# Kernel optimization log

Measured on AMD Instinct MI355X. Metric: run time of the kernel, lower is better.

Reference implementation:

```python
import jax, jax.numpy as jnp
import numpy as np

D_OUT, D_IN, NOBJ, H, A = 12, 2, 8, 256, 100
BN_EPS = 1e-5
N_TOK = 16384  # = 2048 scenes * 8 objects


def _lin(x, W, b=None):
    y = x @ W.T
    return y + b if b is not None else y


def _bn1(x, gamma, beta):
    # BatchNorm1d(num_features=1) in training mode: single channel ->
    # batch statistics are taken over every element of the tensor.
    m = jnp.mean(x)
    v = jnp.var(x)
    return (x - m) * (gamma / jnp.sqrt(v + BN_EPS)) + beta


def _l2norm(x):
    # torch.nn.functional.normalize(dim=-1): x / max(||x||, 1e-12)
    n = jnp.linalg.norm(x, axis=-1, keepdims=True)
    return x / jnp.maximum(n, 1e-12)


def setup_inputs() -> dict:
    key = jax.random.key(0)
    ks = iter(jax.random.split(key, 64))
    def rn(shape, s=1.0):
        return jax.random.normal(next(ks), shape, dtype=jnp.float32) * s
    dx = 2 * (D_OUT + D_IN)       # 28
    df = 2 * (D_OUT + 1 + D_IN)   # 30
    p = 0.05
    return dict(
        z_dyn=rn((N_TOK, D_IN)),
        z_contex=rn((N_TOK, D_OUT)),
        z_mc=rn((N_TOK, 2)),
        W_e=rn((H, dx), p), b_e=rn((H,), p),      # linear_inter
        W_i=rn((H, df), p), b_i=rn((H,), p),      # linear_inter_i
        W_a=rn((H, dx), p), b_a=rn((H,), p),      # linear_inter_a
        W_2=rn((H, H), p), b_2=rn((H,), p),       # linear_inter_2
        W_at=rn((A, H), p), b_at=rn((A,), p),     # linear_att
        W_at2=rn((1, A), p), b_at2=rn((1,), p),   # linear_att_2
        W_s1=rn((H, H), p), b_s1=rn((H,), p),     # linear_S[0]
        W_s2=rn((1, H), p), b_s2=rn((1,), p),     # linear_S[1]
        W_eC=rn((H, df), p), b_eC=rn((H,), p),    # linear_inter_C
        W_iC=rn((H, df), p), b_iC=rn((H,), p),    # linear_inter_i_C
        W_2C=rn((H, H), p), b_2C=rn((H,), p),     # linear_inter_2_C
        W_s1C=rn((H, H), p), b_s1C=rn((H,), p),   # linear_S_C[0]
        W_s2C=rn((1, H), p), b_s2C=rn((1,), p),   # linear_S_C[1]
        g_M=jnp.ones((1,), jnp.float32), be_M=jnp.zeros((1,), jnp.float32),
        g_C=jnp.ones((1,), jnp.float32), be_C=jnp.zeros((1,), jnp.float32),
        W_d=rn((D_IN, H), p),   # dynamic_update (no bias)
        W_dC=rn((D_IN, H), p),  # dynamic_update_C (no bias)
    )


def reference(z_dyn, z_contex, z_mc,
              W_e, b_e, W_i, b_i, W_a, b_a, W_2, b_2,
              W_at, b_at, W_at2, b_at2, W_s1, b_s1, W_s2, b_s2,
              W_eC, b_eC, W_iC, b_iC, W_2C, b_2C,
              W_s1C, b_s1C, W_s2C, b_s2C,
              g_M, be_M, g_C, be_C, W_d, W_dC):
    B = z_dyn.shape[0] // NOBJ
    cd = jnp.concatenate([z_dyn, z_contex], -1).reshape(B, NOBJ, D_IN + D_OUT)
    zm = z_mc[:, 0].reshape(B, NOBJ, 1)
    zc = z_mc[:, 1].reshape(B, NOBJ, 1)
    v = z_dyn.reshape(B, NOBJ, D_IN)
    ct = z_contex.reshape(B, NOBJ, D_OUT)

    def pair(a):
        d = a.shape[-1]
        a1 = jnp.broadcast_to(a[:, None, :, :], (B, NOBJ, NOBJ, d))  # [b,i,j] = a[b,j]
        a2 = jnp.broadcast_to(a[:, :, None, :], (B, NOBJ, NOBJ, d))  # [b,i,j] = a[b,i]
        return a1, a2

    x1, x2 = pair(cd)
    m1, m2 = pair(zm)
    v1, v2 = pair(v)
    ct1, ct2 = pair(ct)
    c1, c2 = pair(zc)

    x_12 = jnp.concatenate([x1, x2], -1)                       # (B,8,8,28)
    f_12 = jnp.concatenate([m1, x1, m2, x2], -1)               # (B,8,8,30)
    fc_12 = jnp.concatenate([ct1, ct2, c1, c2, v1, v2], -1)    # (B,8,8,30)

    E_emb = jax.nn.relu(_lin(x_12, W_e, b_e))
    I_emb = jax.nn.relu(_lin(f_12, W_i, b_i))
    A_emb = jax.nn.relu(_lin(x_12, W_a, b_a))
    E_embC = jax.nn.relu(_lin(fc_12, W_eC, b_eC))
    I_embC = jax.nn.relu(_lin(fc_12, W_iC, b_iC))
    # NOTE: linear_inter_a_C / linear_att_C / linear_att_2_C (presents_C) are
    # dead code in the original forward (computed but never used) -> omitted.

    presents = jax.nn.sigmoid(
        _lin(jnp.tanh(_lin(A_emb, W_at, b_at)), W_at2, b_at2))  # (B,8,8,1)
    mask = (1.0 - jnp.eye(NOBJ, dtype=x_12.dtype))[None, :, :, None]
    pm = presents * mask

    s = _lin(_lin(I_emb, W_s1, b_s1), W_s2, b_s2)               # (B,8,8,1)
    normed = _bn1(s, g_M, be_M)
    scale = (jax.nn.softplus(normed) * pm).sum(axis=1).reshape(B * NOBJ, 1)

    sC = _lin(_lin(I_embC, W_s1C, b_s1C), W_s2C, b_s2C)
    normedC = _bn1(sC, g_C, be_C)
    scaleC = (jax.nn.softplus(normedC) * mask).sum(axis=1).reshape(B * NOBJ, 1)

    E = (_lin(E_emb, W_2, b_2) * pm).sum(axis=1)                # (B,8,256)
    E_C = (_lin(E_embC, W_2C, b_2C) * mask).sum(axis=1)         # (B,8,256)

    nd_mass = scale * _l2norm(_lin(E, W_d).reshape(z_dyn.shape))
    nd_charge = scaleC * _l2norm(_lin(E_C, W_dC).reshape(z_dyn.shape))
    return (nd_mass + nd_charge, nd_mass, nd_charge)
```

## Files before the change

### kernel.cpp

```cpp
#include <hip/hip_runtime.h>
#include <math.h>

#define HDIM 256
#define NATT 100
#define PSTR 260

typedef __attribute__((ext_vector_type(8))) short short8v;
typedef __attribute__((ext_vector_type(4))) float f32x4;

static __device__ __forceinline__ unsigned short f2bf(float x) {
    union { float f; unsigned u; } v; v.f = x;
    const unsigned r = v.u + 0x7FFFu + ((v.u >> 16) & 1u);
    return (unsigned short)(r >> 16);
}
static __device__ __forceinline__ float bf2f(unsigned short s) {
    union { float f; unsigned u; } v; v.u = ((unsigned)s) << 16;
    return v.f;
}

#define WSYNC() do { asm volatile("s_waitcnt lgkmcnt(0)" ::: "memory"); \
                     __builtin_amdgcn_sched_barrier(0); } while (0)

__launch_bounds__(256)
__global__ void prep_kernel(
    const float* __restrict__ Ws1, const float* __restrict__ bs1,
    const float* __restrict__ Ws2, const float* __restrict__ bs2,
    const float* __restrict__ Ws1C, const float* __restrict__ bs1C,
    const float* __restrict__ Ws2C, const float* __restrict__ bs2C,
    const float* __restrict__ W2,  const float* __restrict__ b2,
    const float* __restrict__ Wd,
    const float* __restrict__ W2C, const float* __restrict__ b2C,
    const float* __restrict__ WdC,
    const float* __restrict__ W_at,
    const float* __restrict__ W_a,  const float* __restrict__ b_a,
    const float* __restrict__ W_i,  const float* __restrict__ b_i,
    const float* __restrict__ W_iC, const float* __restrict__ b_iC,
    const float* __restrict__ W_e,  const float* __restrict__ b_e,
    const float* __restrict__ W_eC, const float* __restrict__ b_eC,
    float* __restrict__ wcm, float* __restrict__ wcc,
    float* __restrict__ m2m, float* __restrict__ m2c,
    float* __restrict__ consts, float* __restrict__ stats_acc,
    unsigned short* __restrict__ WtH, unsigned short* __restrict__ WtL,
    unsigned short* __restrict__ WcH, unsigned short* __restrict__ WcL)
{
    const int tid = threadIdx.x;
    const int blk = blockIdx.x;
    if (blk < 4) {
        const int h = blk*64 + (tid>>2), l = tid&3;
        float a = 0.f;
        for (int k = l*64; k < l*64 + 64; ++k) a += Ws2[k] * Ws1[k*HDIM + h];
        a += __shfl_xor(a, 1); a += __shfl_xor(a, 2);
        if (l == 0) wcm[h] = a;
    } else if (blk < 8) {
        const int h = (blk-4)*64 + (tid>>2), l = tid&3;
        float a = 0.f;
        for (int k = l*64; k < l*64 + 64; ++k) a += Ws2C[k] * Ws1C[k*HDIM + h];
        a += __shfl_xor(a, 1); a += __shfl_xor(a, 2);
        if (l == 0) wcc[h] = a;
    } else if (blk < 16) {
        const int idx = (blk-8)*64 + (tid>>2), l = tid&3;
        const int c = idx >> 8, h = idx & 255;
        float a = 0.f;
        for (int k = l*64; k < l*64 + 64; ++k) a += Wd[c*HDIM + k] * W2[k*HDIM + h];
        a += __shfl_xor(a, 1); a += __shfl_xor(a, 2);
        if (l == 0) m2m[c*HDIM + h] = a;
    } else if (blk < 24) {
        const int idx = (blk-16)*64 + (tid>>2), l = tid&3;
        const int c = idx >> 8, h = idx & 255;
        float a = 0.f;
        for (int k = l*64; k < l*64 + 64; ++k) a += WdC[c*HDIM + k] * W2C[k*HDIM + h];
        a += __shfl_xor(a, 1); a += __shfl_xor(a, 2);
        if (l == 0) m2c[c*HDIM + h] = a;
    } else if (blk == 24) {
        __shared__ float red[6][4];
        const int k = tid;
        float p[6];
        p[0] = Ws2[k]  * bs1[k];
        p[1] = Ws2C[k] * bs1C[k];
        p[2] = Wd[k]        * b2[k];
        p[3] = Wd[HDIM+k]   * b2[k];
        p[4] = WdC[k]       * b2C[k];
        p[5] = WdC[HDIM+k]  * b2C[k];
        #pragma unroll
        for (int m = 1; m < 64; m <<= 1) {
            #pragma unroll
            for (int q = 0; q < 6; ++q) p[q] += __shfl_xor(p[q], m);
        }
        if ((tid & 63) == 0) {
            const int wv = tid >> 6;
            #pragma unroll
            for (int q = 0; q < 6; ++q) red[q][wv] = p[q];
        }
        __syncthreads();
        if (tid == 0) {
            float c0 = bs2[0], c1 = bs2C[0], c2 = 0, c3 = 0, c4 = 0, c5 = 0;
            for (int q = 0; q < 4; ++q) {
                c0 += red[0][q]; c1 += red[1][q]; c2 += red[2][q];
                c3 += red[3][q]; c4 += red[4][q]; c5 += red[5][q];
            }
            consts[0] = c0; consts[1] = c1; consts[2] = c2;
            consts[3] = c3; consts[4] = c4; consts[5] = c5;
            stats_acc[0] = 0.f; stats_acc[1] = 0.f;
            stats_acc[2] = 0.f; stats_acc[3] = 0.f;
        }
    } else if (blk < 33) {
        const int rbase = (blk - 25) * 14;
        const int h = tid;
        for (int rr = 0; rr < 14; ++rr) {
            const int row = rbase + rr;
            const float v = (row < NATT) ? W_at[row*HDIM + h] : 0.f;
            const int n = row >> 4, lr = row & 15;
            const int kk = h >> 5, kc = h & 31;
            const int idx = ((n*8 + kk)*16 + lr)*32 + kc;
            const unsigned short hi = f2bf(v);
            WtH[idx] = hi;
            WtL[idx] = f2bf(v - bf2f(hi));
        }
    } else {
        const int q = blk - 33;
        const int m = q >> 1, x = q & 1;
        const int h = tid;
        const float* W; const float* bias; int type;
        switch (m) {
            case 0:  W = W_a;  bias = b_a;  type = 0; break;
            case 1:  W = W_i;  bias = b_i;  type = 1; break;
            case 2:  W = W_iC; bias = b_iC; type = 2; break;
            case 3:  W = W_e;  bias = b_e;  type = 0; break;
            default: W = W_eC; bias = b_eC; type = 2; break;
        }
        float tmp[32];
        #pragma unroll
        for (int k = 0; k < 32; ++k) tmp[k] = 0.f;
        if (type == 0) {
            const float* row = W + h*28 + x*14;
            for (int k = 0; k < 14; ++k) tmp[k] = row[k];
        } else if (type == 1) {
            const float* row = W + h*30 + x*15;
            tmp[14] = row[0];
            for (int k = 0; k < 14; ++k) tmp[k] = row[1+k];
        } else {
            const float* row = W + h*30;
            for (int k = 0; k < 12; ++k) tmp[2+k] = row[x*12 + k];
            tmp[15] = row[24 + x];
            tmp[0] = row[26 + x*2];
            tmp[1] = row[27 + x*2];
        }
        tmp[16] = 0.5f * bias[h];
        const int base = (q*HDIM + h)*32;
        for (int k = 0; k < 32; ++k) {
            const unsigned short hi = f2bf(tmp[k]);
            WcH[base + k] = hi;
            WcL[base + k] = f2bf(tmp[k] - bf2f(hi));
        }
    }
}

__launch_bounds__(256, 2)
__global__ void main_kernel(
    const float* __restrict__ z_dyn, const float* __restrict__ z_contex,
    const float* __restrict__ z_mc,
    const float* __restrict__ b_at,
    const float* __restrict__ W_at2, const float* __restrict__ b_at2,
    const unsigned short* __restrict__ WtH, const unsigned short* __restrict__ WtL,
    const unsigned short* __restrict__ WcH, const unsigned short* __restrict__ WcL,
    const float* __restrict__ wcm,  const float* __restrict__ wcc,
    const float* __restrict__ m2m,  const float* __restrict__ m2c,
    const float* __restrict__ consts,
    float* __restrict__ pm_g, float* __restrict__ s_g, float* __restrict__ sC_g,
    float* __restrict__ um_g, float* __restrict__ uc_g,
    float* __restrict__ stats_acc, int nscene)
{
    __shared__ float s_in[4][8][16];
    alignas(16) __shared__ float proj[4][16][PSTR];
    __shared__ float pm_t[4][64];
    __shared__ float pmsum[4][8];

    const int tid  = threadIdx.x;
    const int w    = tid >> 6;
    const int lane = tid & 63;
    const int lr   = lane & 15;
    const int lq   = lane >> 4;
    const int scene = blockIdx.x*4 + w;
    if (scene >= nscene) return;

    {
        const int o = lane >> 3, c = lane & 7;
        const int tok = scene*8 + o;
        const float v0 = (c < 2) ? z_dyn[tok*2 + c] : z_contex[tok*12 + (c-2)];
        const int c2 = c + 8;
        const float v1 = (c2 < 14) ? z_contex[tok*12 + (c2-2)] : z_mc[tok*2 + (c2-14)];
        s_in[w][o][c]  = v0;
        s_in[w][o][c2] = v1;
    }
    WSYNC();

    short8v bfh, bfl;
    #pragma unroll
    for (int e = 0; e < 8; ++e) {
        const int k = lq*8 + e;
        float f = 0.f;
        if (lr < 8) f = (k < 16) ? s_in[w][lr][k] : (k == 16 ? 1.0f : 0.f);
        const unsigned short h16 = f2bf(f);
        bfh[e] = (short)h16;
        bfl[e] = (short)f2bf(f - bf2f(h16));
    }

#define PROJECT(MIDX)                                                          \
    {                                                                          \
        const int mb2 = (MIDX)*2*HDIM*32;                                      \
        _Pragma("unroll 4")                                                    \
        for (int jj = 0; jj < 32; ++jj) {                                      \
            const int x = jj >> 4, t = jj & 15;                                \
            const int off = mb2 + ((x*HDIM) + t*16 + lr)*32 + lq*8;            \
            const short8v ah = *(const short8v*)&WcH[off];                     \
            const short8v al = *(const short8v*)&WcL[off];                     \
            f32x4 d = (f32x4){0.f, 0.f, 0.f, 0.f};                             \
            d = __builtin_amdgcn_mfma_f32_16x16x32_bf16(ah, bfh, d, 0, 0, 0);  \
            d = __builtin_amdgcn_mfma_f32_16x16x32_bf16(al, bfh, d, 0, 0, 0);  \
            d = __builtin_amdgcn_mfma_f32_16x16x32_bf16(ah, bfl, d, 0, 0, 0);  \
            if (lr < 8) *(f32x4*)&proj[w][x*8 + lr][t*16 + lq*4] = d;          \
        }                                                                      \
    }                                                                          \
    WSYNC();

    PROJECT(0)
    {
        f32x4 acc[7][4];
        #pragma unroll
        for (int n = 0; n < 7; ++n)
            #pragma unroll
            for (int pt = 0; pt < 4; ++pt) acc[n][pt] = (f32x4){0.f,0.f,0.f,0.f};

        #pragma unroll 2
        for (int k = 0; k < 8; ++k) {
            const int kb = k*32 + lq*8;
            short8v pfh[4], pfl[4];
            #pragma unroll
            for (int pt = 0; pt < 4; ++pt) {
                const int p = pt*16 + lr;
                const int jA = p & 7, iA = p >> 3;
                const float4 vj0 = *(const float4*)&proj[w][jA][kb];
                const float4 vj1 = *(const float4*)&proj[w][jA][kb+4];
                const float4 vi0 = *(const float4*)&proj[w][8+iA][kb];
                const float4 vi1 = *(const float4*)&proj[w][8+iA][kb+4];
                const float v[8] = {vj0.x+vi0.x, vj0.y+vi0.y, vj0.z+vi0.z, vj0.w+vi0.w,
                                    vj1.x+vi1.x, vj1.y+vi1.y, vj1.z+vi1.z, vj1.w+vi1.w};
                #pragma unroll
                for (int e = 0; e < 8; ++e) {
                    const float r = fmaxf(v[e], 0.f);
                    const unsigned short h16 = f2bf(r);
                    pfh[pt][e] = (short)h16;
                    pfl[pt][e] = (short)f2bf(r - bf2f(h16));
                }
            }
            #pragma unroll
            for (int n = 0; n < 7; ++n) {
                const int wo = (n*8 + k)*512 + lr*32 + lq*8;
                const short8v wh = *(const short8v*)&WtH[wo];
                const short8v wl = *(const short8v*)&WtL[wo];
                #pragma unroll
                for (int pt = 0; pt < 4; ++pt) {
                    acc[n][pt] = __builtin_amdgcn_mfma_f32_16x16x32_bf16(wh, pfh[pt], acc[n][pt], 0, 0, 0);
                    acc[n][pt] = __builtin_amdgcn_mfma_f32_16x16x32_bf16(wl, pfh[pt], acc[n][pt], 0, 0, 0);
                    acc[n][pt] = __builtin_amdgcn_mfma_f32_16x16x32_bf16(wh, pfl[pt], acc[n][pt], 0, 0, 0);
                }
            }
        }
        float part[4] = {0.f, 0.f, 0.f, 0.f};
        #pragma unroll
        for (int n = 0; n < 7; ++n) {
            #pragma unroll
            for (int r = 0; r < 4; ++r) {
                const int a = 16*n + lq*4 + r;
                if (a < NATT) {
                    const float bat = b_at[a], w2 = W_at2[a];
                    #pragma unroll
                    for (int pt = 0; pt < 4; ++pt)
                        part[pt] += w2 * tanhf(acc[n][pt][r] + bat);
                }
            }
        }
        #pragma unroll
        for (int pt = 0; pt < 4; ++pt) {
            float s = part[pt];
            s += __shfl_xor(s, 16); s += __shfl_xor(s, 32);
            part[pt] = s;
        }
        if (lq == 0) {
            const float b2v = b_at2[0];
            #pragma unroll
            for (int pt = 0; pt < 4; ++pt) {
                const int p = pt*16 + lr;
                const int ip = p >> 3, jp = p & 7;
                const float pres = 1.f / (1.f + expf(-(part[pt] + b2v)));
                const float pmv = (ip != jp) ? pres : 0.f;
                pm_t[w][jp*8 + ip] = pmv;
                pm_g[scene*64 + jp*8 + ip] = pmv;
            }
        }
    }
    WSYNC();
    if (lane < 8) {
        const float4 q0 = *(const float4*)&pm_t[w][lane*8];
        const float4 q1 = *(const float4*)&pm_t[w][lane*8 + 4];
        pmsum[w][lane] = q0.x+q0.y+q0.z+q0.w + q1.x+q1.y+q1.z+q1.w;
    }
    WSYNC();

    const int jp = lane >> 3, ip = lane & 7;
    float sv, svC;

    PROJECT(1)
    {
        float a = 0.f;
        #pragma unroll 8
        for (int u = 0; u < 64; ++u) {
            const int h4 = u*4;
            const float4 aj = *(const float4*)&proj[w][jp][h4];
            const float4 ai = *(const float4*)&proj[w][8+ip][h4];
            const float4 wv = *(const float4*)&wcm[h4];
            a += wv.x*fmaxf(aj.x+ai.x, 0.f) + wv.y*fmaxf(aj.y+ai.y, 0.f)
               + wv.z*fmaxf(aj.z+ai.z, 0.f) + wv.w*fmaxf(aj.w+ai.w, 0.f);
        }
        sv = a + consts[0];
        s_g[scene*64 + lane] = sv;
    }
    WSYNC();

    PROJECT(2)
    {
        float a = 0.f;
        #pragma unroll 8
        for (int u = 0; u < 64; ++u) {
            const int h4 = u*4;
            const float4 aj = *(const float4*)&proj[w][jp][h4];
            const float4 ai = *(const float4*)&proj[w][8+ip][h4];
            const float4 wv = *(const float4*)&wcc[h4];
            a += wv.x*fmaxf(aj.x+ai.x, 0.f) + wv.y*fmaxf(aj.y+ai.y, 0.f)
               + wv.z*fmaxf(aj.z+ai.z, 0.f) + wv.w*fmaxf(aj.w+ai.w, 0.f);
        }
        svC = a + consts[1];
        sC_g[scene*64 + lane] = svC;
    }
    WSYNC();

    {
        float a0 = sv, a1 = sv*sv, a2 = svC, a3 = svC*svC;
        #pragma unroll
        for (int m = 1; m < 64; m <<= 1) {
            a0 += __shfl_xor(a0, m); a1 += __shfl_xor(a1, m);
            a2 += __shfl_xor(a2, m); a3 += __shfl_xor(a3, m);
        }
        if (lane == 0) {
            atomicAdd(&stats_acc[0], a0); atomicAdd(&stats_acc[1], a1);
            atomicAdd(&stats_acc[2], a2); atomicAdd(&stats_acc[3], a3);
        }
    }

    PROJECT(3)
    {
        float p0 = 0.f, p1 = 0.f;
        #pragma unroll 8
        for (int u = 0; u < 64; ++u) {
            const int h4 = u*4;
            const float4 aj = *(const float4*)&proj[w][jp][h4];
            const float4 ai = *(const float4*)&proj[w][8+ip][h4];
            const float4 m0 = *(const float4*)&m2m[h4];
            const float4 m1 = *(const float4*)&m2m[HDIM + h4];
            const float e0 = fmaxf(aj.x+ai.x, 0.f), e1 = fmaxf(aj.y+ai.y, 0.f);
            const float e2 = fmaxf(aj.z+ai.z, 0.f), e3 = fmaxf(aj.w+ai.w, 0.f);
            p0 += m0.x*e0 + m0.y*e1 + m0.z*e2 + m0.w*e3;
            p1 += m1.x*e0 + m1.y*e1 + m1.z*e2 + m1.w*e3;
        }
        const float pmv = pm_t[w][jp*8 + ip];
        p0 *= pmv; p1 *= pmv;
        p0 += __shfl_xor(p0, 1); p0 += __shfl_xor(p0, 2); p0 += __shfl_xor(p0, 4);
        p1 += __shfl_xor(p1, 1); p1 += __shfl_xor(p1, 2); p1 += __shfl_xor(p1, 4);
        if (ip == 0) {
            const float ps = pmsum[w][jp];
            const float y0 = p0 + ps*consts[2];
            const float y1 = p1 + ps*consts[3];
            const float nrm = fmaxf(sqrtf(y0*y0 + y1*y1), 1e-12f);
            *(float2*)&um_g[(scene*8 + jp)*2] = make_float2(y0/nrm, y1/nrm);
        }
    }
    WSYNC();

    PROJECT(4)
    {
        float p0 = 0.f, p1 = 0.f;
        #pragma unroll 8
        for (int u = 0; u < 64; ++u) {
            const int h4 = u*4;
            const float4 aj = *(const float4*)&proj[w][jp][h4];
            const float4 ai = *(const float4*)&proj[w][8+ip][h4];
            const float4 m0 = *(const float4*)&m2c[h4];
            const float4 m1 = *(const float4*)&m2c[HDIM + h4];
            const float e0 = fmaxf(aj.x+ai.x, 0.f), e1 = fmaxf(aj.y+ai.y, 0.f);
            const float e2 = fmaxf(aj.z+ai.z, 0.f), e3 = fmaxf(aj.w+ai.w, 0.f);
            p0 += m0.x*e0 + m0.y*e1 + m0.z*e2 + m0.w*e3;
            p1 += m1.x*e0 + m1.y*e1 + m1.z*e2 + m1.w*e3;
        }
        const float mk = (ip != jp) ? 1.f : 0.f;
        p0 *= mk; p1 *= mk;
        p0 += __shfl_xor(p0, 1); p0 += __shfl_xor(p0, 2); p0 += __shfl_xor(p0, 4);
        p1 += __shfl_xor(p1, 1); p1 += __shfl_xor(p1, 2); p1 += __shfl_xor(p1, 4);
        if (ip == 0) {
            const float y0 = p0 + 7.0f*consts[4];
            const float y1 = p1 + 7.0f*consts[5];
            const float nrm = fmaxf(sqrtf(y0*y0 + y1*y1), 1e-12f);
            *(float2*)&uc_g[(scene*8 + jp)*2] = make_float2(y0/nrm, y1/nrm);
        }
    }
#undef PROJECT
}

__launch_bounds__(256)
__global__ void final_kernel(const float* __restrict__ s_g, const float* __restrict__ sC_g,
                             const float* __restrict__ pm_g,
                             const float* __restrict__ um_g, const float* __restrict__ uc_g,
                             const float* __restrict__ stats_acc,
                             const float* __restrict__ gM, const float* __restrict__ beM,
                             const float* __restrict__ gC, const float* __restrict__ beC,
                             float* __restrict__ out, int ntok, float inv_n)
{
    const int t = blockIdx.x * blockDim.x + threadIdx.x;
    if (t >= ntok) return;
    const int j = t & 7;
    float mean = stats_acc[0] * inv_n;
    float var  = stats_acc[1] * inv_n - mean*mean;
    const float kM = gM[0] / sqrtf(var + 1e-5f);
    const float cM = beM[0] - mean*kM;
    mean = stats_acc[2] * inv_n;
    var  = stats_acc[3] * inv_n - mean*mean;
    const float kC = gC[0] / sqrtf(var + 1e-5f);
    const float cC = beC[0] - mean*kC;

    const float4 sa = *(const float4*)&s_g[t*8];
    const float4 sb = *(const float4*)&s_g[t*8 + 4];
    const float4 ca = *(const float4*)&sC_g[t*8];
    const float4 cb = *(const float4*)&sC_g[t*8 + 4];
    const float4 pa = *(const float4*)&pm_g[t*8];
    const float4 pb = *(const float4*)&pm_g[t*8 + 4];
    const float sv[8] = {sa.x,sa.y,sa.z,sa.w, sb.x,sb.y,sb.z,sb.w};
    const float cv[8] = {ca.x,ca.y,ca.z,ca.w, cb.x,cb.y,cb.z,cb.w};
    const float pv[8] = {pa.x,pa.y,pa.z,pa.w, pb.x,pb.y,pb.z,pb.w};
    float sc = 0.f, scC = 0.f, spj = 0.f;
    #pragma unroll
    for (int i = 0; i < 8; ++i) {
        const float sn = sv[i]*kM + cM;
        const float sp = fmaxf(sn, 0.f) + log1pf(expf(-fabsf(sn)));
        sc += sp * pv[i];
        const float snc = cv[i]*kC + cC;
        const float spc = fmaxf(snc, 0.f) + log1pf(expf(-fabsf(snc)));
        scC += spc;
        if (i == j) spj = spc;
    }
    scC -= spj;
    const float2 u_m = *(const float2*)&um_g[t*2];
    const float2 u_c = *(const float2*)&uc_g[t*2];
    const float m0 = sc  * u_m.x, m1 = sc  * u_m.y;
    const float c0 = scC * u_c.x, c1 = scC * u_c.y;
    *(float2*)&out[t*2]          = make_float2(m0 + c0, m1 + c1);
    *(float2*)&out[ntok*2 + t*2] = make_float2(m0, m1);
    *(float2*)&out[ntok*4 + t*2] = make_float2(c0, c1);
}

extern "C" void kernel_launch(void* const* d_in, const int* in_sizes, int n_in,
                              void* d_out, int out_size, void* d_ws, size_t ws_size,
                              hipStream_t stream) {
    const float* z_dyn    = (const float*)d_in[0];
    const float* z_contex = (const float*)d_in[1];
    const float* z_mc     = (const float*)d_in[2];
    const float* W_e   = (const float*)d_in[3];  const float* b_e   = (const float*)d_in[4];
    const float* W_i   = (const float*)d_in[5];  const float* b_i   = (const float*)d_in[6];
    const float* W_a   = (const float*)d_in[7];  const float* b_a   = (const float*)d_in[8];
    const float* W_2   = (const float*)d_in[9];  const float* b_2   = (const float*)d_in[10];
    const float* W_at  = (const float*)d_in[11]; const float* b_at  = (const float*)d_in[12];
    const float* W_at2 = (const float*)d_in[13]; const float* b_at2 = (const float*)d_in[14];
    const float* W_s1  = (const float*)d_in[15]; const float* b_s1  = (const float*)d_in[16];
    const float* W_s2  = (const float*)d_in[17]; const float* b_s2  = (const float*)d_in[18];
    const float* W_eC  = (const float*)d_in[19]; const float* b_eC  = (const float*)d_in[20];
    const float* W_iC  = (const float*)d_in[21]; const float* b_iC  = (const float*)d_in[22];
    const float* W_2C  = (const float*)d_in[23]; const float* b_2C  = (const float*)d_in[24];
    const float* W_s1C = (const float*)d_in[25]; const float* b_s1C = (const float*)d_in[26];
    const float* W_s2C = (const float*)d_in[27]; const float* b_s2C = (const float*)d_in[28];
    const float* g_M   = (const float*)d_in[29]; const float* be_M  = (const float*)d_in[30];
    const float* g_C   = (const float*)d_in[31]; const float* be_C  = (const float*)d_in[32];
    const float* W_d   = (const float*)d_in[33];
    const float* W_dC  = (const float*)d_in[34];

    const int ntok = in_sizes[0] / 2;
    const int B = ntok / 8;

    float* ws = (float*)d_ws;
    float* pm_g   = ws;
    float* s_g    = pm_g + B*64;
    float* sC_g   = s_g  + B*64;
    float* um_g   = sC_g + B*64;
    float* uc_g   = um_g + ntok*2;
    float* wcm    = uc_g + ntok*2;
    float* wcc    = wcm + 256;
    float* m2m    = wcc + 256;
    float* m2c    = m2m + 512;
    float* consts = m2c + 512;
    float* stats_acc = consts + 8;
    unsigned short* WtH = (unsigned short*)(stats_acc + 4);
    unsigned short* WtL = WtH + 7*8*512;
    unsigned short* WcH = WtL + 7*8*512;
    unsigned short* WcL = WcH + 10*HDIM*32;

    prep_kernel<<<43, 256, 0, stream>>>(
        W_s1, b_s1, W_s2, b_s2, W_s1C, b_s1C, W_s2C, b_s2C,
        W_2, b_2, W_d, W_2C, b_2C, W_dC, W_at,
        W_a, b_a, W_i, b_i, W_iC, b_iC, W_e, b_e, W_eC, b_eC,
        wcm, wcc, m2m, m2c, consts, stats_acc, WtH, WtL, WcH, WcL);

    main_kernel<<<(B + 3)/4, 256, 0, stream>>>(
        z_dyn, z_contex, z_mc,
        b_at, W_at2, b_at2,
        WtH, WtL, WcH, WcL,
        wcm, wcc, m2m, m2c, consts,
        pm_g, s_g, sC_g, um_g, uc_g, stats_acc, B);

    final_kernel<<<(ntok + 255)/256, 256, 0, stream>>>(
        s_g, sC_g, pm_g, um_g, uc_g, stats_acc,
        g_M, be_M, g_C, be_C,
        (float*)d_out, ntok, 1.0f / (float)(B*64));
}
```

Baseline: 347.1 us.

## Fuse main and final kernels with a grid-wide barrier and re-split work per block

Merges the main and final kernels into a single persistent launch of 1024 blocks. Each block processes two scenes with all four waves cooperating per scene, instead of one wave per scene. Per-scene intermediates stay in shared memory rather than going through global workspace. BatchNorm statistics are accumulated into 16 spread atomic slots, followed by an atomic-counter grid barrier before each block computes its outputs. It also adds fast tanh/sigmoid helpers and raises launch bounds to 4 blocks per CU. This removes one launch and the global round-trip, but the design relies on all 1024 blocks being co-resident and adds spin-wait latency.

```diff
diff --git a/kernel.cpp b/kernel.cpp
--- a/kernel.cpp
+++ b/kernel.cpp
@@ -3,7 +3,7 @@
 
 #define HDIM 256
 #define NATT 100
-#define PSTR 260
+#define NBLK2 1024
 
 typedef __attribute__((ext_vector_type(8))) short short8v;
 typedef __attribute__((ext_vector_type(4))) float f32x4;
@@ -17,116 +17,114 @@
     union { float f; unsigned u; } v; v.u = ((unsigned)s) << 16;
     return v.f;
 }
-
-#define WSYNC() do { asm volatile("s_waitcnt lgkmcnt(0)" ::: "memory"); \
-                     __builtin_amdgcn_sched_barrier(0); } while (0)
+static __device__ __forceinline__ float fast_tanh(float x) {
+    const float e = __builtin_amdgcn_exp2f(x * 2.885390081777927f);
+    return 1.f - 2.f * __builtin_amdgcn_rcpf(e + 1.f);
+}
+static __device__ __forceinline__ float fast_sigmoid(float x) {
+    const float e = __builtin_amdgcn_exp2f(-x * 1.4426950408889634f);
+    return __builtin_amdgcn_rcpf(1.f + e);
+}
+
+struct Params {
+    const float *z_dyn, *z_contex, *z_mc;
+    const float *b_at, *W_at2, *b_at2;
+    const float *Ws1, *bs1, *Ws2, *bs2, *Ws1C, *bs1C, *Ws2C, *bs2C;
+    const float *W2, *b2, *Wd, *W2C, *b2C, *WdC, *W_at;
+    const float *W_a, *b_a, *W_i, *b_i, *W_iC, *b_iC, *W_e, *b_e, *W_eC, *b_eC;
+    const float *g_M, *be_M, *g_C, *be_C;
+    float *wcm, *wcc, *m2m, *m2c, *consts, *stats_acc;
+    unsigned int *bar;
+    unsigned short *WtH, *WtL, *WcH, *WcL;
+    float *out;
+    int nscene, ntok;
+    float inv_n;
+};
 
 __launch_bounds__(256)
-__global__ void prep_kernel(
-    const float* __restrict__ Ws1, const float* __restrict__ bs1,
-    const float* __restrict__ Ws2, const float* __restrict__ bs2,
-    const float* __restrict__ Ws1C, const float* __restrict__ bs1C,
-    const float* __restrict__ Ws2C, const float* __restrict__ bs2C,
-    const float* __restrict__ W2,  const float* __restrict__ b2,
-    const float* __restrict__ Wd,
-    const float* __restrict__ W2C, const float* __restrict__ b2C,
-    const float* __restrict__ WdC,
-    const float* __restrict__ W_at,
-    const float* __restrict__ W_a,  const float* __restrict__ b_a,
-    const float* __restrict__ W_i,  const float* __restrict__ b_i,
-    const float* __restrict__ W_iC, const float* __restrict__ b_iC,
-    const float* __restrict__ W_e,  const float* __restrict__ b_e,
-    const float* __restrict__ W_eC, const float* __restrict__ b_eC,
-    float* __restrict__ wcm, float* __restrict__ wcc,
-    float* __restrict__ m2m, float* __restrict__ m2c,
-    float* __restrict__ consts, float* __restrict__ stats_acc,
-    unsigned short* __restrict__ WtH, unsigned short* __restrict__ WtL,
-    unsigned short* __restrict__ WcH, unsigned short* __restrict__ WcL)
+__global__ void prep_kernel(Params P)
 {
     const int tid = threadIdx.x;
     const int blk = blockIdx.x;
+    __shared__ float red[6][4];
     if (blk < 4) {
         const int h = blk*64 + (tid>>2), l = tid&3;
         float a = 0.f;
-        for (int k = l*64; k < l*64 + 64; ++k) a += Ws2[k] * Ws1[k*HDIM + h];
+        for (int k = l*64; k < l*64 + 64; ++k) a += P.Ws2[k] * P.Ws1[k*HDIM + h];
         a += __shfl_xor(a, 1); a += __shfl_xor(a, 2);
-        if (l == 0) wcm[h] = a;
+        if (l == 0) P.wcm[h] = a;
     } else if (blk < 8) {
         const int h = (blk-4)*64 + (tid>>2), l = tid&3;
         float a = 0.f;
-        for (int k = l*64; k < l*64 + 64; ++k) a += Ws2C[k] * Ws1C[k*HDIM + h];
+        for (int k = l*64; k < l*64 + 64; ++k) a += P.Ws2C[k] * P.Ws1C[k*HDIM + h];
         a += __shfl_xor(a, 1); a += __shfl_xor(a, 2);
-        if (l == 0) wcc[h] = a;
+        if (l == 0) P.wcc[h] = a;
     } else if (blk < 16) {
         const int idx = (blk-8)*64 + (tid>>2), l = tid&3;
         const int c = idx >> 8, h = idx & 255;
         float a = 0.f;
-        for (int k = l*64; k < l*64 + 64; ++k) a += Wd[c*HDIM + k] * W2[k*HDIM + h];
+        for (int k = l*64; k < l*64 + 64; ++k) a += P.Wd[c*HDIM + k] * P.W2[k*HDIM + h];
         a += __shfl_xor(a, 1); a += __shfl_xor(a, 2);
-        if (l == 0) m2m[c*HDIM + h] = a;
+        if (l == 0) P.m2m[c*HDIM + h] = a;
     } else if (blk < 24) {
         const int idx = (blk-16)*64 + (tid>>2), l = tid&3;
         const int c = idx >> 8, h = idx & 255;
         float a = 0.f;
-        for (int k = l*64; k < l*64 + 64; ++k) a += WdC[c*HDIM + k] * W2C[k*HDIM + h];
+        for (int k = l*64; k < l*64 + 64; ++k) a += P.WdC[c*HDIM + k] * P.W2C[k*HDIM + h];
         a += __shfl_xor(a, 1); a += __shfl_xor(a, 2);
-        if (l == 0) m2c[c*HDIM + h] = a;
+        if (l == 0) P.m2c[c*HDIM + h] = a;
     } else if (blk == 24) {
-        __shared__ float red[6][4];
         const int k = tid;
         float p[6];
-        p[0] = Ws2[k]  * bs1[k];
-        p[1] = Ws2C[k] * bs1C[k];
-        p[2] = Wd[k]        * b2[k];
-        p[3] = Wd[HDIM+k]   * b2[k];
-        p[4] = WdC[k]       * b2C[k];
-        p[5] = WdC[HDIM+k]  * b2C[k];
+        p[0] = P.Ws2[k]       * P.bs1[k];
+        p[1] = P.Ws2C[k]      * P.bs1C[k];
+        p[2] = P.Wd[k]        * P.b2[k];
+        p[3] = P.Wd[HDIM+k]   * P.b2[k];
+        p[4] = P.WdC[k]       * P.b2C[k];
+        p[5] = P.WdC[HDIM+k]  * P.b2C[k];
         #pragma unroll
         for (int m = 1; m < 64; m <<= 1) {
             #pragma unroll
             for (int q = 0; q < 6; ++q) p[q] += __shfl_xor(p[q], m);
         }
         if ((tid & 63) == 0) {
-            const int wv = tid >> 6;
-            #pragma unroll
-            for (int q = 0; q < 6; ++q) red[q][wv] = p[q];
+            #pragma unroll
+            for (int q = 0; q < 6; ++q) red[q][tid>>6] = p[q];
         }
         __syncthreads();
         if (tid == 0) {
-            float c0 = bs2[0], c1 = bs2C[0], c2 = 0, c3 = 0, c4 = 0, c5 = 0;
+            float c0 = P.bs2[0], c1 = P.bs2C[0], c2 = 0, c3 = 0, c4 = 0, c5 = 0;
             for (int q = 0; q < 4; ++q) {
                 c0 += red[0][q]; c1 += red[1][q]; c2 += red[2][q];
                 c3 += red[3][q]; c4 += red[4][q]; c5 += red[5][q];
             }
-            consts[0] = c0; consts[1] = c1; consts[2] = c2;
-            consts[3] = c3; consts[4] = c4; consts[5] = c5;
-            stats_acc[0] = 0.f; stats_acc[1] = 0.f;
-            stats_acc[2] = 0.f; stats_acc[3] = 0.f;
+            P.consts[0] = c0; P.consts[1] = c1; P.consts[2] = c2;
+            P.consts[3] = c3; P.consts[4] = c4; P.consts[5] = c5;
         }
     } else if (blk < 33) {
         const int rbase = (blk - 25) * 14;
         const int h = tid;
         for (int rr = 0; rr < 14; ++rr) {
             const int row = rbase + rr;
-            const float v = (row < NATT) ? W_at[row*HDIM + h] : 0.f;
-            const int n = row >> 4, lr = row & 15;
+            const float v = (row < NATT) ? P.W_at[row*HDIM + h] : 0.f;
+            const int n = row >> 4, r16 = row & 15;
             const int kk = h >> 5, kc = h & 31;
-            const int idx = ((n*8 + kk)*16 + lr)*32 + kc;
+            const int idx = ((n*8 + kk)*16 + r16)*32 + kc;
             const unsigned short hi = f2bf(v);
-            WtH[idx] = hi;
-            WtL[idx] = f2bf(v - bf2f(hi));
-        }
-    } else {
+            P.WtH[idx] = hi;
+            P.WtL[idx] = f2bf(v - bf2f(hi));
+        }
+    } else if (blk < 43) {
         const int q = blk - 33;
         const int m = q >> 1, x = q & 1;
         const int h = tid;
         const float* W; const float* bias; int type;
         switch (m) {
-            case 0:  W = W_a;  bias = b_a;  type = 0; break;
-            case 1:  W = W_i;  bias = b_i;  type = 1; break;
-            case 2:  W = W_iC; bias = b_iC; type = 2; break;
-            case 3:  W = W_e;  bias = b_e;  type = 0; break;
-            default: W = W_eC; bias = b_eC; type = 2; break;
+            case 0:  W = P.W_a;  bias = P.b_a;  type = 0; break;
+            case 1:  W = P.W_i;  bias = P.b_i;  type = 1; break;
+            case 2:  W = P.W_iC; bias = P.b_iC; type = 2; break;
+            case 3:  W = P.W_e;  bias = P.b_e;  type = 0; break;
+            default: W = P.W_eC; bias = P.b_eC; type = 2; break;
         }
         float tmp[32];
         #pragma unroll
@@ -149,382 +147,365 @@
         const int base = (q*HDIM + h)*32;
         for (int k = 0; k < 32; ++k) {
             const unsigned short hi = f2bf(tmp[k]);
-            WcH[base + k] = hi;
-            WcL[base + k] = f2bf(tmp[k] - bf2f(hi));
-        }
+            P.WcH[base + k] = hi;
+            P.WcL[base + k] = f2bf(tmp[k] - bf2f(hi));
+        }
+    } else {
+        if (tid < 64) P.stats_acc[tid] = 0.f;
+        if (tid == 64) P.bar[0] = 0u;
     }
 }
 
-__launch_bounds__(256, 2)
-__global__ void main_kernel(
-    const float* __restrict__ z_dyn, const float* __restrict__ z_contex,
-    const float* __restrict__ z_mc,
-    const float* __restrict__ b_at,
-    const float* __restrict__ W_at2, const float* __restrict__ b_at2,
-    const unsigned short* __restrict__ WtH, const unsigned short* __restrict__ WtL,
-    const unsigned short* __restrict__ WcH, const unsigned short* __restrict__ WcL,
-    const float* __restrict__ wcm,  const float* __restrict__ wcc,
-    const float* __restrict__ m2m,  const float* __restrict__ m2c,
-    const float* __restrict__ consts,
-    float* __restrict__ pm_g, float* __restrict__ s_g, float* __restrict__ sC_g,
-    float* __restrict__ um_g, float* __restrict__ uc_g,
-    float* __restrict__ stats_acc, int nscene)
+__launch_bounds__(256, 4)
+__global__ void main_final_kernel(Params P)
 {
-    __shared__ float s_in[4][8][16];
-    alignas(16) __shared__ float proj[4][16][PSTR];
-    __shared__ float pm_t[4][64];
-    __shared__ float pmsum[4][8];
+    __shared__ float s_in[8][16];
+    alignas(16) __shared__ float proj[16][260];
+    __shared__ float pm2[2][64];
+    __shared__ float pmsum2[2][8];
+    __shared__ float ss2[2][64];
+    __shared__ float sq2[2][64];
+    __shared__ float y_s[16], y2_s[16];
+    __shared__ float um2[2][8][2], uc2[2][8][2];
+    __shared__ float stf[4];
 
     const int tid  = threadIdx.x;
-    const int w    = tid >> 6;
+    const int blk  = blockIdx.x;
     const int lane = tid & 63;
+    const int lw   = tid >> 6;
     const int lr   = lane & 15;
     const int lq   = lane >> 4;
-    const int scene = blockIdx.x*4 + w;
-    if (scene >= nscene) return;
-
-    {
-        const int o = lane >> 3, c = lane & 7;
-        const int tok = scene*8 + o;
-        const float v0 = (c < 2) ? z_dyn[tok*2 + c] : z_contex[tok*12 + (c-2)];
-        const int c2 = c + 8;
-        const float v1 = (c2 < 14) ? z_contex[tok*12 + (c2-2)] : z_mc[tok*2 + (c2-14)];
-        s_in[w][o][c]  = v0;
-        s_in[w][o][c2] = v1;
-    }
-    WSYNC();
-
-    short8v bfh, bfl;
-    #pragma unroll
-    for (int e = 0; e < 8; ++e) {
-        const int k = lq*8 + e;
-        float f = 0.f;
-        if (lr < 8) f = (k < 16) ? s_in[w][lr][k] : (k == 16 ? 1.0f : 0.f);
-        const unsigned short h16 = f2bf(f);
-        bfh[e] = (short)h16;
-        bfl[e] = (short)f2bf(f - bf2f(h16));
-    }
+
+    const float c0 = P.consts[0], c1 = P.consts[1], c2 = P.consts[2];
+    const float c3 = P.consts[3], c4 = P.consts[4], c5 = P.consts[5];
+
+    float b0 = 0.f, b1 = 0.f, b2a = 0.f, b3 = 0.f;
 
 #define PROJECT(MIDX)                                                          \
     {                                                                          \
         const int mb2 = (MIDX)*2*HDIM*32;                                      \
-        _Pragma("unroll 4")                                                    \
-        for (int jj = 0; jj < 32; ++jj) {                                      \
-            const int x = jj >> 4, t = jj & 15;                                \
+        _Pragma("unroll")                                                      \
+        for (int jj = 0; jj < 8; ++jj) {                                       \
+            const int job = lw*8 + jj;                                         \
+            const int x = job >> 4, t = job & 15;                              \
             const int off = mb2 + ((x*HDIM) + t*16 + lr)*32 + lq*8;            \
-            const short8v ah = *(const short8v*)&WcH[off];                     \
-            const short8v al = *(const short8v*)&WcL[off];                     \
+            const short8v ah = *(const short8v*)&P.WcH[off];                   \
+            const short8v al = *(const short8v*)&P.WcL[off];                   \
             f32x4 d = (f32x4){0.f, 0.f, 0.f, 0.f};                             \
             d = __builtin_amdgcn_mfma_f32_16x16x32_bf16(ah, bfh, d, 0, 0, 0);  \
             d = __builtin_amdgcn_mfma_f32_16x16x32_bf16(al, bfh, d, 0, 0, 0);  \
             d = __builtin_amdgcn_mfma_f32_16x16x32_bf16(ah, bfl, d, 0, 0, 0);  \
-            if (lr < 8) *(f32x4*)&proj[w][x*8 + lr][t*16 + lq*4] = d;          \
+            if (lr < 8) *(f32x4*)&proj[x*8 + lr][t*16 + lq*4] = d;             \
         }                                                                      \
     }                                                                          \
-    WSYNC();
-
-    PROJECT(0)
-    {
-        f32x4 acc[7][4];
+    __syncthreads();
+
+    for (int sc = 0; sc < 2; ++sc) {
+        const int scene = blk*2 + sc;
+        __syncthreads();
+
+        if (tid < 128) {
+            const int o = tid >> 4, c = tid & 15;
+            const int tok = scene*8 + o;
+            float v;
+            if (c < 2)       v = P.z_dyn[tok*2 + c];
+            else if (c < 14) v = P.z_contex[tok*12 + (c-2)];
+            else             v = P.z_mc[tok*2 + (c-14)];
+            s_in[o][c] = v;
+        }
+        __syncthreads();
+
+        short8v bfh, bfl;
         #pragma unroll
-        for (int n = 0; n < 7; ++n)
-            #pragma unroll
-            for (int pt = 0; pt < 4; ++pt) acc[n][pt] = (f32x4){0.f,0.f,0.f,0.f};
-
-        #pragma unroll 2
-        for (int k = 0; k < 8; ++k) {
-            const int kb = k*32 + lq*8;
-            short8v pfh[4], pfl[4];
-            #pragma unroll
-            for (int pt = 0; pt < 4; ++pt) {
-                const int p = pt*16 + lr;
-                const int jA = p & 7, iA = p >> 3;
-                const float4 vj0 = *(const float4*)&proj[w][jA][kb];
-                const float4 vj1 = *(const float4*)&proj[w][jA][kb+4];
-                const float4 vi0 = *(const float4*)&proj[w][8+iA][kb];
-                const float4 vi1 = *(const float4*)&proj[w][8+iA][kb+4];
+        for (int e = 0; e < 8; ++e) {
+            const int k = lq*8 + e;
+            float f = 0.f;
+            if (lr < 8) f = (k < 16) ? s_in[lr][k] : (k == 16 ? 1.0f : 0.f);
+            const unsigned short h16 = f2bf(f);
+            bfh[e] = (short)h16;
+            bfl[e] = (short)f2bf(f - bf2f(h16));
+        }
+
+        PROJECT(0)
+        {
+            const int p = lw*16 + lr;
+            const int jA = p & 7, iA = p >> 3;
+            f32x4 acc[7];
+            #pragma unroll
+            for (int n = 0; n < 7; ++n) acc[n] = (f32x4){0.f, 0.f, 0.f, 0.f};
+
+            #pragma unroll 2
+            for (int k = 0; k < 8; ++k) {
+                const int kb = k*32 + lq*8;
+                const float4 vj0 = *(const float4*)&proj[jA][kb];
+                const float4 vj1 = *(const float4*)&proj[jA][kb+4];
+                const float4 vi0 = *(const float4*)&proj[8+iA][kb];
+                const float4 vi1 = *(const float4*)&proj[8+iA][kb+4];
                 const float v[8] = {vj0.x+vi0.x, vj0.y+vi0.y, vj0.z+vi0.z, vj0.w+vi0.w,
                                     vj1.x+vi1.x, vj1.y+vi1.y, vj1.z+vi1.z, vj1.w+vi1.w};
+                short8v pfh, pfl;
                 #pragma unroll
                 for (int e = 0; e < 8; ++e) {
                     const float r = fmaxf(v[e], 0.f);
                     const unsigned short h16 = f2bf(r);
-                    pfh[pt][e] = (short)h16;
-                    pfl[pt][e] = (short)f2bf(r - bf2f(h16));
+                    pfh[e] = (short)h16;
+                    pfl[e] = (short)f2bf(r - bf2f(h16));
                 }
-            }
+                #pragma unroll
+                for (int n = 0; n < 7; ++n) {
+                    const int wo = (n*8 + k)*512 + lr*32 + lq*8;
+                    const short8v wh = *(const short8v*)&P.WtH[wo];
+                    const short8v wl = *(const short8v*)&P.WtL[wo];
+                    acc[n] = __builtin_amdgcn_mfma_f32_16x16x32_bf16(wh, pfh, acc[n], 0, 0, 0);
+                    acc[n] = __builtin_amdgcn_mfma_f32_16x16x32_bf16(wl, pfh, acc[n], 0, 0, 0);
+                    acc[n] = __builtin_amdgcn_mfma_f32_16x16x32_bf16(wh, pfl, acc[n], 0, 0, 0);
+                }
+            }
+            float part = 0.f;
             #pragma unroll
             for (int n = 0; n < 7; ++n) {
-                const int wo = (n*8 + k)*512 + lr*32 + lq*8;
-                const short8v wh = *(const short8v*)&WtH[wo];
-                const short8v wl = *(const short8v*)&WtL[wo];
                 #pragma unroll
-                for (int pt = 0; pt < 4; ++pt) {
-                    acc[n][pt] = __builtin_amdgcn_mfma_f32_16x16x32_bf16(wh, pfh[pt], acc[n][pt], 0, 0, 0);
-                    acc[n][pt] = __builtin_amdgcn_mfma_f32_16x16x32_bf16(wl, pfh[pt], acc[n][pt], 0, 0, 0);
-                    acc[n][pt] = __builtin_amdgcn_mfma_f32_16x16x32_bf16(wh, pfl[pt], acc[n][pt], 0, 0, 0);
+                for (int r = 0; r < 4; ++r) {
+                    const int a = 16*n + lq*4 + r;
+                    if (a < NATT)
+                        part += P.W_at2[a] * fast_tanh(acc[n][r] + P.b_at[a]);
                 }
             }
-        }
-        float part[4] = {0.f, 0.f, 0.f, 0.f};
-        #pragma unroll
-        for (int n = 0; n < 7; ++n) {
-            #pragma unroll
-            for (int r = 0; r < 4; ++r) {
-                const int a = 16*n + lq*4 + r;
-                if (a < NATT) {
-                    const float bat = b_at[a], w2 = W_at2[a];
-                    #pragma unroll
-                    for (int pt = 0; pt < 4; ++pt)
-                        part[pt] += w2 * tanhf(acc[n][pt][r] + bat);
-                }
-            }
-        }
-        #pragma unroll
-        for (int pt = 0; pt < 4; ++pt) {
-            float s = part[pt];
-            s += __shfl_xor(s, 16); s += __shfl_xor(s, 32);
-            part[pt] = s;
-        }
-        if (lq == 0) {
-            const float b2v = b_at2[0];
-            #pragma unroll
-            for (int pt = 0; pt < 4; ++pt) {
-                const int p = pt*16 + lr;
+            part += __shfl_xor(part, 16); part += __shfl_xor(part, 32);
+            if (lq == 0) {
                 const int ip = p >> 3, jp = p & 7;
-                const float pres = 1.f / (1.f + expf(-(part[pt] + b2v)));
-                const float pmv = (ip != jp) ? pres : 0.f;
-                pm_t[w][jp*8 + ip] = pmv;
-                pm_g[scene*64 + jp*8 + ip] = pmv;
-            }
-        }
-    }
-    WSYNC();
-    if (lane < 8) {
-        const float4 q0 = *(const float4*)&pm_t[w][lane*8];
-        const float4 q1 = *(const float4*)&pm_t[w][lane*8 + 4];
-        pmsum[w][lane] = q0.x+q0.y+q0.z+q0.w + q1.x+q1.y+q1.z+q1.w;
-    }
-    WSYNC();
-
-    const int jp = lane >> 3, ip = lane & 7;
-    float sv, svC;
-
-    PROJECT(1)
-    {
-        float a = 0.f;
-        #pragma unroll 8
-        for (int u = 0; u < 64; ++u) {
-            const int h4 = u*4;
-            const float4 aj = *(const float4*)&proj[w][jp][h4];
-            const float4 ai = *(const float4*)&proj[w][8+ip][h4];
-            const float4 wv = *(const float4*)&wcm[h4];
-            a += wv.x*fmaxf(aj.x+ai.x, 0.f) + wv.y*fmaxf(aj.y+ai.y, 0.f)
-               + wv.z*fmaxf(aj.z+ai.z, 0.f) + wv.w*fmaxf(aj.w+ai.w, 0.f);
-        }
-        sv = a + consts[0];
-        s_g[scene*64 + lane] = sv;
-    }
-    WSYNC();
-
-    PROJECT(2)
-    {
-        float a = 0.f;
-        #pragma unroll 8
-        for (int u = 0; u < 64; ++u) {
-            const int h4 = u*4;
-            const float4 aj = *(const float4*)&proj[w][jp][h4];
-            const float4 ai = *(const float4*)&proj[w][8+ip][h4];
-            const float4 wv = *(const float4*)&wcc[h4];
-            a += wv.x*fmaxf(aj.x+ai.x, 0.f) + wv.y*fmaxf(aj.y+ai.y, 0.f)
-               + wv.z*fmaxf(aj.z+ai.z, 0.f) + wv.w*fmaxf(aj.w+ai.w, 0.f);
-        }
-        svC = a + consts[1];
-        sC_g[scene*64 + lane] = svC;
-    }
-    WSYNC();
-
-    {
-        float a0 = sv, a1 = sv*sv, a2 = svC, a3 = svC*svC;
-        #pragma unroll
-        for (int m = 1; m < 64; m <<= 1) {
-            a0 += __shfl_xor(a0, m); a1 += __shfl_xor(a1, m);
-            a2 += __shfl_xor(a2, m); a3 += __shfl_xor(a3, m);
-        }
-        if (lane == 0) {
-            atomicAdd(&stats_acc[0], a0); atomicAdd(&stats_acc[1], a1);
-            atomicAdd(&stats_acc[2], a2); atomicAdd(&stats_acc[3], a3);
-        }
-    }
-
-    PROJECT(3)
-    {
-        float p0 = 0.f, p1 = 0.f;
-        #pragma unroll 8
-        for (int u = 0; u < 64; ++u) {
-            const int h4 = u*4;
-            const float4 aj = *(const float4*)&proj[w][jp][h4];
-            const float4 ai = *(const float4*)&proj[w][8+ip][h4];
-            const float4 m0 = *(const float4*)&m2m[h4];
-            const float4 m1 = *(const float4*)&m2m[HDIM + h4];
-            const float e0 = fmaxf(aj.x+ai.x, 0.f), e1 = fmaxf(aj.y+ai.y, 0.f);
-            const float e2 = fmaxf(aj.z+ai.z, 0.f), e3 = fmaxf(aj.w+ai.w, 0.f);
-            p0 += m0.x*e0 + m0.y*e1 + m0.z*e2 + m0.w*e3;
-            p1 += m1.x*e0 + m1.y*e1 + m1.z*e2 + m1.w*e3;
-        }
-        const float pmv = pm_t[w][jp*8 + ip];
-        p0 *= pmv; p1 *= pmv;
-        p0 += __shfl_xor(p0, 1); p0 += __shfl_xor(p0, 2); p0 += __shfl_xor(p0, 4);
-        p1 += __shfl_xor(p1, 1); p1 += __shfl_xor(p1, 2); p1 += __shfl_xor(p1, 4);
-        if (ip == 0) {
-            const float ps = pmsum[w][jp];
-            const float y0 = p0 + ps*consts[2];
-            const float y1 = p1 + ps*consts[3];
-            const float nrm = fmaxf(sqrtf(y0*y0 + y1*y1), 1e-12f);
-            *(float2*)&um_g[(scene*8 + jp)*2] = make_float2(y0/nrm, y1/nrm);
-        }
-    }
-    WSYNC();
-
-    PROJECT(4)
-    {
-        float p0 = 0.f, p1 = 0.f;
-        #pragma unroll 8
-        for (int u = 0; u < 64; ++u) {
-            const int h4 = u*4;
-            const float4 aj = *(const float4*)&proj[w][jp][h4];
-            const float4 ai = *(const float4*)&proj[w][8+ip][h4];
-            const float4 m0 = *(const float4*)&m2c[h4];
-            const float4 m1 = *(const float4*)&m2c[HDIM + h4];
-            const float e0 = fmaxf(aj.x+ai.x, 0.f), e1 = fmaxf(aj.y+ai.y, 0.f);
-            const float e2 = fmaxf(aj.z+ai.z, 0.f), e3 = fmaxf(aj.w+ai.w, 0.f);
-            p0 += m0.x*e0 + m0.y*e1 + m0.z*e2 + m0.w*e3;
-            p1 += m1.x*e0 + m1.y*e1 + m1.z*e2 + m1.w*e3;
-        }
-        const float mk = (ip != jp) ? 1.f : 0.f;
-        p0 *= mk; p1 *= mk;
-        p0 += __shfl_xor(p0, 1); p0 += __shfl_xor(p0, 2); p0 += __shfl_xor(p0, 4);
-        p1 += __shfl_xor(p1, 1); p1 += __shfl_xor(p1, 2); p1 += __shfl_xor(p1, 4);
-        if (ip == 0) {
-            const float y0 = p0 + 7.0f*consts[4];
-            const float y1 = p1 + 7.0f*consts[5];
-            const float nrm = fmaxf(sqrtf(y0*y0 + y1*y1), 1e-12f);
-            *(float2*)&uc_g[(scene*8 + jp)*2] = make_float2(y0/nrm, y1/nrm);
+                const float pres = fast_sigmoid(part + P.b_at2[0]);
+                pm2[sc][jp*8 + ip] = (ip != jp) ? pres : 0.f;
+            }
+        }
+        __syncthreads();
+        if (tid < 8) {
+            const float4 q0 = *(const float4*)&pm2[sc][tid*8];
+            const float4 q1 = *(const float4*)&pm2[sc][tid*8 + 4];
+            pmsum2[sc][tid] = q0.x+q0.y+q0.z+q0.w + q1.x+q1.y+q1.z+q1.w;
+        }
+
+        const int q   = tid >> 2, l2 = tid & 3;
+        const int jp2 = q >> 3, ip2 = q & 7;
+
+        PROJECT(1)
+        {
+            float a = 0.f;
+            #pragma unroll
+            for (int u = 0; u < 16; ++u) {
+                const int h4 = (l2*16 + u) * 4;
+                const float4 aj = *(const float4*)&proj[jp2][h4];
+                const float4 ai = *(const float4*)&proj[8+ip2][h4];
+                const float4 wv = *(const float4*)&P.wcm[h4];
+                a += wv.x*fmaxf(aj.x+ai.x, 0.f) + wv.y*fmaxf(aj.y+ai.y, 0.f)
+                   + wv.z*fmaxf(aj.z+ai.z, 0.f) + wv.w*fmaxf(aj.w+ai.w, 0.f);
+            }
+            a += __shfl_xor(a, 1); a += __shfl_xor(a, 2);
+            if (l2 == 0) ss2[sc][q] = a + c0;
+        }
+        __syncthreads();
+
+        PROJECT(2)
+        {
+            float a = 0.f;
+            #pragma unroll
+            for (int u = 0; u < 16; ++u) {
+                const int h4 = (l2*16 + u) * 4;
+                const float4 aj = *(const float4*)&proj[jp2][h4];
+                const float4 ai = *(const float4*)&proj[8+ip2][h4];
+                const float4 wv = *(const float4*)&P.wcc[h4];
+                a += wv.x*fmaxf(aj.x+ai.x, 0.f) + wv.y*fmaxf(aj.y+ai.y, 0.f)
+                   + wv.z*fmaxf(aj.z+ai.z, 0.f) + wv.w*fmaxf(aj.w+ai.w, 0.f);
+            }
+            a += __shfl_xor(a, 1); a += __shfl_xor(a, 2);
+            if (l2 == 0) sq2[sc][q] = a + c1;
+        }
+        __syncthreads();
+
+        if (tid < 64) {
+            const float v1 = ss2[sc][tid], v2 = sq2[sc][tid];
+            float a0 = v1, a1 = v1*v1, a2 = v2, a3 = v2*v2;
+            #pragma unroll
+            for (int m = 1; m < 64; m <<= 1) {
+                a0 += __shfl_xor(a0, m); a1 += __shfl_xor(a1, m);
+                a2 += __shfl_xor(a2, m); a3 += __shfl_xor(a3, m);
+            }
+            b0 += a0; b1 += a1; b2a += a2; b3 += a3;
+        }
+
+        PROJECT(3)
+        {
+            float p0 = 0.f, p1 = 0.f;
+            #pragma unroll
+            for (int u = 0; u < 16; ++u) {
+                const int h4 = (l2*16 + u) * 4;
+                const float4 aj = *(const float4*)&proj[jp2][h4];
+                const float4 ai = *(const float4*)&proj[8+ip2][h4];
+                const float4 m0 = *(const float4*)&P.m2m[h4];
+                const float4 m1 = *(const float4*)&P.m2m[HDIM + h4];
+                const float e0 = fmaxf(aj.x+ai.x, 0.f), e1 = fmaxf(aj.y+ai.y, 0.f);
+                const float e2 = fmaxf(aj.z+ai.z, 0.f), e3 = fmaxf(aj.w+ai.w, 0.f);
+                p0 += m0.x*e0 + m0.y*e1 + m0.z*e2 + m0.w*e3;
+                p1 += m1.x*e0 + m1.y*e1 + m1.z*e2 + m1.w*e3;
+            }
+            p0 += __shfl_xor(p0, 1); p0 += __shfl_xor(p0, 2);
+            p1 += __shfl_xor(p1, 1); p1 += __shfl_xor(p1, 2);
+            const float pmv = pm2[sc][q];
+            p0 *= pmv; p1 *= pmv;
+            p0 += __shfl_xor(p0, 4); p0 += __shfl_xor(p0, 8); p0 += __shfl_xor(p0, 16);
+            p1 += __shfl_xor(p1, 4); p1 += __shfl_xor(p1, 8); p1 += __shfl_xor(p1, 16);
+            if ((tid & 31) == 0) {
+                y_s[(tid>>5)*2 + 0] = p0;
+                y_s[(tid>>5)*2 + 1] = p1;
+            }
+        }
+        __syncthreads();
+
+        PROJECT(4)
+        {
+            float p0 = 0.f, p1 = 0.f;
+            #pragma unroll
+            for (int u = 0; u < 16; ++u) {
+                const int h4 = (l2*16 + u) * 4;
+                const float4 aj = *(const float4*)&proj[jp2][h4];
+                const float4 ai = *(const float4*)&proj[8+ip2][h4];
+                const float4 m0 = *(const float4*)&P.m2c[h4];
+                const float4 m1 = *(const float4*)&P.m2c[HDIM + h4];
+                const float e0 = fmaxf(aj.x+ai.x, 0.f), e1 = fmaxf(aj.y+ai.y, 0.f);
+                const float e2 = fmaxf(aj.z+ai.z, 0.f), e3 = fmaxf(aj.w+ai.w, 0.f);
+                p0 += m0.x*e0 + m0.y*e1 + m0.z*e2 + m0.w*e3;
+                p1 += m1.x*e0 + m1.y*e1 + m1.z*e2 + m1.w*e3;
+            }
+            p0 += __shfl_xor(p0, 1); p0 += __shfl_xor(p0, 2);
+            p1 += __shfl_xor(p1, 1); p1 += __shfl_xor(p1, 2);
+            const float mk = (ip2 != jp2) ? 1.f : 0.f;
+            p0 *= mk; p1 *= mk;
+            p0 += __shfl_xor(p0, 4); p0 += __shfl_xor(p0, 8); p0 += __shfl_xor(p0, 16);
+            p1 += __shfl_xor(p1, 4); p1 += __shfl_xor(p1, 8); p1 += __shfl_xor(p1, 16);
+            if ((tid & 31) == 0) {
+                y2_s[(tid>>5)*2 + 0] = p0;
+                y2_s[(tid>>5)*2 + 1] = p1;
+            }
+        }
+        __syncthreads();
+
+        if (tid < 16) {
+            const int type = tid >> 3, j = tid & 7;
+            float yy0, yy1;
+            if (type == 0) {
+                const float ps = pmsum2[sc][j];
+                yy0 = y_s[j*2]     + ps*c2;
+                yy1 = y_s[j*2 + 1] + ps*c3;
+            } else {
+                yy0 = y2_s[j*2]     + 7.0f*c4;
+                yy1 = y2_s[j*2 + 1] + 7.0f*c5;
+            }
+            const float nrm = fmaxf(sqrtf(yy0*yy0 + yy1*yy1), 1e-12f);
+            if (type == 0) { um2[sc][j][0] = yy0/nrm; um2[sc][j][1] = yy1/nrm; }
+            else           { uc2[sc][j][0] = yy0/nrm; uc2[sc][j][1] = yy1/nrm; }
         }
     }
 #undef PROJECT
-}
-
-__launch_bounds__(256)
-__global__ void final_kernel(const float* __restrict__ s_g, const float* __restrict__ sC_g,
-                             const float* __restrict__ pm_g,
-                             const float* __restrict__ um_g, const float* __restrict__ uc_g,
-                             const float* __restrict__ stats_acc,
-                             const float* __restrict__ gM, const float* __restrict__ beM,
-                             const float* __restrict__ gC, const float* __restrict__ beC,
-                             float* __restrict__ out, int ntok, float inv_n)
-{
-    const int t = blockIdx.x * blockDim.x + threadIdx.x;
-    if (t >= ntok) return;
-    const int j = t & 7;
-    float mean = stats_acc[0] * inv_n;
-    float var  = stats_acc[1] * inv_n - mean*mean;
-    const float kM = gM[0] / sqrtf(var + 1e-5f);
-    const float cM = beM[0] - mean*kM;
-    mean = stats_acc[2] * inv_n;
-    var  = stats_acc[3] * inv_n - mean*mean;
-    const float kC = gC[0] / sqrtf(var + 1e-5f);
-    const float cC = beC[0] - mean*kC;
-
-    const float4 sa = *(const float4*)&s_g[t*8];
-    const float4 sb = *(const float4*)&s_g[t*8 + 4];
-    const float4 ca = *(const float4*)&sC_g[t*8];
-    const float4 cb = *(const float4*)&sC_g[t*8 + 4];
-    const float4 pa = *(const float4*)&pm_g[t*8];
-    const float4 pb = *(const float4*)&pm_g[t*8 + 4];
-    const float sv[8] = {sa.x,sa.y,sa.z,sa.w, sb.x,sb.y,sb.z,sb.w};
-    const float cv[8] = {ca.x,ca.y,ca.z,ca.w, cb.x,cb.y,cb.z,cb.w};
-    const float pv[8] = {pa.x,pa.y,pa.z,pa.w, pb.x,pb.y,pb.z,pb.w};
-    float sc = 0.f, scC = 0.f, spj = 0.f;
-    #pragma unroll
-    for (int i = 0; i < 8; ++i) {
-        const float sn = sv[i]*kM + cM;
-        const float sp = fmaxf(sn, 0.f) + log1pf(expf(-fabsf(sn)));
-        sc += sp * pv[i];
-        const float snc = cv[i]*kC + cC;
-        const float spc = fmaxf(snc, 0.f) + log1pf(expf(-fabsf(snc)));
-        scC += spc;
-        if (i == j) spj = spc;
+
+    if (tid == 0) {
+        float* slot = P.stats_acc + (blk & 15)*4;
+        atomicAdd(&slot[0], b0); atomicAdd(&slot[1], b1);
+        atomicAdd(&slot[2], b2a); atomicAdd(&slot[3], b3);
+        __threadfence();
+        __hip_atomic_fetch_add(P.bar, 1u, __ATOMIC_ACQ_REL, __HIP_MEMORY_SCOPE_AGENT);
+        while (__hip_atomic_load(P.bar, __ATOMIC_ACQUIRE, __HIP_MEMORY_SCOPE_AGENT) < (unsigned)NBLK2)
+            __builtin_amdgcn_s_sleep(8);
     }
-    scC -= spj;
-    const float2 u_m = *(const float2*)&um_g[t*2];
-    const float2 u_c = *(const float2*)&uc_g[t*2];
-    const float m0 = sc  * u_m.x, m1 = sc  * u_m.y;
-    const float c0 = scC * u_c.x, c1 = scC * u_c.y;
-    *(float2*)&out[t*2]          = make_float2(m0 + c0, m1 + c1);
-    *(float2*)&out[ntok*2 + t*2] = make_float2(m0, m1);
-    *(float2*)&out[ntok*4 + t*2] = make_float2(c0, c1);
+    __syncthreads();
+
+    if (tid < 64) {
+        float v = __hip_atomic_load(&P.stats_acc[tid], __ATOMIC_RELAXED,
+                                    __HIP_MEMORY_SCOPE_AGENT);
+        v += __shfl_xor(v, 4); v += __shfl_xor(v, 8);
+        v += __shfl_xor(v, 16); v += __shfl_xor(v, 32);
+        if (tid < 4) stf[tid] = v;
+    }
+    __syncthreads();
+
+    if (tid < 16) {
+        float mean = stf[0] * P.inv_n;
+        float var  = stf[1] * P.inv_n - mean*mean;
+        const float kM = P.g_M[0] / sqrtf(var + 1e-5f);
+        const float cM = P.be_M[0] - mean*kM;
+        mean = stf[2] * P.inv_n;
+        var  = stf[3] * P.inv_n - mean*mean;
+        const float kC = P.g_C[0] / sqrtf(var + 1e-5f);
+        const float cC = P.be_C[0] - mean*kC;
+
+        const int sc = tid >> 3, j = tid & 7;
+        const int t = (blk*2 + sc)*8 + j;
+        float sum_m = 0.f, sum_c = 0.f;
+        #pragma unroll
+        for (int i = 0; i < 8; ++i) {
+            const int idx = j*8 + i;
+            const float sn = ss2[sc][idx]*kM + cM;
+            const float sp = fmaxf(sn, 0.f) + log1pf(expf(-fabsf(sn)));
+            sum_m += sp * pm2[sc][idx];
+            const float snc = sq2[sc][idx]*kC + cC;
+            const float spc = fmaxf(snc, 0.f) + log1pf(expf(-fabsf(snc)));
+            sum_c += (i != j) ? spc : 0.f;
+        }
+        const float m0 = sum_m * um2[sc][j][0], m1 = sum_m * um2[sc][j][1];
+        const float q0 = sum_c * uc2[sc][j][0], q1 = sum_c * uc2[sc][j][1];
+        float* out = P.out;
+        const int ntok = P.ntok;
+        *(float2*)&out[t*2]          = make_float2(m0 + q0, m1 + q1);
+        *(float2*)&out[ntok*2 + t*2] = make_float2(m0, m1);
+        *(float2*)&out[ntok*4 + t*2] = make_float2(q0, q1);
+    }
 }
 
 extern "C" void kernel_launch(void* const* d_in, const int* in_sizes, int n_in,
                               void* d_out, int out_size, void* d_ws, size_t ws_size,
                               hipStream_t stream) {
-    const float* z_dyn    = (const float*)d_in[0];
-    const float* z_contex = (const float*)d_in[1];
-    const float* z_mc     = (const float*)d_in[2];
-    const float* W_e   = (const float*)d_in[3];  const float* b_e   = (const float*)d_in[4];
-    const float* W_i   = (const float*)d_in[5];  const float* b_i   = (const float*)d_in[6];
-    const float* W_a   = (const float*)d_in[7];  const float* b_a   = (const float*)d_in[8];
-    const float* W_2   = (const float*)d_in[9];  const float* b_2   = (const float*)d_in[10];
-    const float* W_at  = (const float*)d_in[11]; const float* b_at  = (const float*)d_in[12];
-    const float* W_at2 = (const float*)d_in[13]; const float* b_at2 = (const float*)d_in[14];
-    const float* W_s1  = (const float*)d_in[15]; const float* b_s1  = (const float*)d_in[16];
-    const float* W_s2  = (const float*)d_in[17]; const float* b_s2  = (const float*)d_in[18];
-    const float* W_eC  = (const float*)d_in[19]; const float* b_eC  = (const float*)d_in[20];
-    const float* W_iC  = (const float*)d_in[21]; const float* b_iC  = (const float*)d_in[22];
-    const float* W_2C  = (const float*)d_in[23]; const float* b_2C  = (const float*)d_in[24];
-    const float* W_s1C = (const float*)d_in[25]; const float* b_s1C = (const float*)d_in[26];
-    const float* W_s2C = (const float*)d_in[27]; const float* b_s2C = (const float*)d_in[28];
-    const float* g_M   = (const float*)d_in[29]; const float* be_M  = (const float*)d_in[30];
-    const float* g_C   = (const float*)d_in[31]; const float* be_C  = (const float*)d_in[32];
-    const float* W_d   = (const float*)d_in[33];
-    const float* W_dC  = (const float*)d_in[34];
+    Params P;
+    P.z_dyn    = (const float*)d_in[0];
+    P.z_contex = (const float*)d_in[1];
+    P.z_mc     = (const float*)d_in[2];
+    P.W_e   = (const float*)d_in[3];  P.b_e   = (const float*)d_in[4];
+    P.W_i   = (const float*)d_in[5];  P.b_i   = (const float*)d_in[6];
+    P.W_a   = (const float*)d_in[7];  P.b_a   = (const float*)d_in[8];
+    P.W2    = (const float*)d_in[9];  P.b2    = (const float*)d_in[10];
+    P.W_at  = (const float*)d_in[11]; P.b_at  = (const float*)d_in[12];
+    P.W_at2 = (const float*)d_in[13]; P.b_at2 = (const float*)d_in[14];
+    P.Ws1   = (const float*)d_in[15]; P.bs1   = (const float*)d_in[16];
+    P.Ws2   = (const float*)d_in[17]; P.bs2   = (const float*)d_in[18];
+    P.W_eC  = (const float*)d_in[19]; P.b_eC  = (const float*)d_in[20];
+    P.W_iC  = (const float*)d_in[21]; P.b_iC  = (const float*)d_in[22];
+    P.W2C   = (const float*)d_in[23]; P.b2C   = (const float*)d_in[24];
+    P.Ws1C  = (const float*)d_in[25]; P.bs1C  = (const float*)d_in[26];
+    P.Ws2C  = (const float*)d_in[27]; P.bs2C  = (const float*)d_in[28];
+    P.g_M   = (const float*)d_in[29]; P.be_M  = (const float*)d_in[30];
+    P.g_C   = (const float*)d_in[31]; P.be_C  = (const float*)d_in[32];
+    P.Wd    = (const float*)d_in[33];
+    P.WdC   = (const float*)d_in[34];
 
     const int ntok = in_sizes[0] / 2;
     const int B = ntok / 8;
 
     float* ws = (float*)d_ws;
-    float* pm_g   = ws;
-    float* s_g    = pm_g + B*64;
-    float* sC_g   = s_g  + B*64;
-    float* um_g   = sC_g + B*64;
-    float* uc_g   = um_g + ntok*2;
-    float* wcm    = uc_g + ntok*2;
-    float* wcc    = wcm + 256;
-    float* m2m    = wcc + 256;
-    float* m2c    = m2m + 512;
-    float* consts = m2c + 512;
-    float* stats_acc = consts + 8;
-    unsigned short* WtH = (unsigned short*)(stats_acc + 4);
-    unsigned short* WtL = WtH + 7*8*512;
-    unsigned short* WcH = WtL + 7*8*512;
-    unsigned short* WcL = WcH + 10*HDIM*32;
-
-    prep_kernel<<<43, 256, 0, stream>>>(
-        W_s1, b_s1, W_s2, b_s2, W_s1C, b_s1C, W_s2C, b_s2C,
-        W_2, b_2, W_d, W_2C, b_2C, W_dC, W_at,
-        W_a, b_a, W_i, b_i, W_iC, b_iC, W_e, b_e, W_eC, b_eC,
-        wcm, wcc, m2m, m2c, consts, stats_acc, WtH, WtL, WcH, WcL);
-
-    main_kernel<<<(B + 3)/4, 256, 0, stream>>>(
-        z_dyn, z_contex, z_mc,
-        b_at, W_at2, b_at2,
-        WtH, WtL, WcH, WcL,
-        wcm, wcc, m2m, m2c, consts,
-        pm_g, s_g, sC_g, um_g, uc_g, stats_acc, B);
-
-    final_kernel<<<(ntok + 255)/256, 256, 0, stream>>>(
-        s_g, sC_g, pm_g, um_g, uc_g, stats_acc,
-        g_M, be_M, g_C, be_C,
-        (float*)d_out, ntok, 1.0f / (float)(B*64));
-}
+    P.wcm    = ws;
+    P.wcc    = P.wcm + 256;
+    P.m2m    = P.wcc + 256;
+    P.m2c    = P.m2m + 512;
+    P.consts = P.m2c + 512;
+    P.stats_acc = P.consts + 8;
+    P.bar    = (unsigned int*)(P.stats_acc + 64);
+    unsigned short* WtH = (unsigned short*)((float*)P.bar + 4);
+    P.WtH = WtH;
+    P.WtL = WtH + 7*8*512;
+    P.WcH = P.WtL + 7*8*512;
+    P.WcL = P.WcH + 10*HDIM*32;
+    P.out = (float*)d_out;
+    P.nscene = B;
+    P.ntok = ntok;
+    P.inv_n = 1.0f / (float)(B*64);
+
+    prep_kernel<<<44, 256, 0, stream>>>(P);
+    main_final_kernel<<<NBLK2, 256, 0, stream>>>(P);
+}
```

Measured after the change: 722.9 us. 2.08x slower.
